# Kernel optimization log

Measured on AMD Instinct MI355X. Metric: run time of the kernel, lower is better.

The kernel has to match this reference:

```python
import jax, jax.numpy as jnp
import numpy as np

WINDOW = 128
CAUSAL = True
LOOK_BACKWARD = 1
LOOK_FORWARD = 0  # causal forces look_forward = 0


def _look_around(x, backward, forward, pad_value, dim):
    # pad along window axis (axis=1), then concat shifted slices along `dim`
    nw = x.shape[1]
    pad_cfg = [(0, 0)] * x.ndim
    pad_cfg[1] = (backward, forward)
    padded = jnp.pad(x, pad_cfg, constant_values=pad_value)
    slices = [padded[:, i:i + nw] for i in range(forward + backward + 1)]
    return jnp.concatenate(slices, axis=dim)


def setup_inputs() -> dict:
    key = jax.random.key(0)
    kq, kk, kv = jax.random.split(key, 3)
    shape = (2, 16, 4096, 64)
    return {
        "q": jax.random.normal(kq, shape, dtype=jnp.float32),
        "k": jax.random.normal(kk, shape, dtype=jnp.float32),
        "v": jax.random.normal(kv, shape, dtype=jnp.float32),
    }


def reference(q, k, v):
    b, h, t, e = q.shape
    scale = e ** (-0.5)
    windows = t // WINDOW  # t assumed divisible by WINDOW (pad_to_multiple is no-op)

    # merge batch and heads, bucket into windows
    bq = q.reshape(b * h, windows, WINDOW, e)
    bk = k.reshape(b * h, windows, WINDOW, e)
    bv = v.reshape(b * h, windows, WINDOW, e)

    # look-around gather of key/value windows: j-dim = WINDOW*(1+back+fwd)
    bk = _look_around(bk, LOOK_BACKWARD, LOOK_FORWARD, 0.0, dim=2)
    bv = _look_around(bv, LOOK_BACKWARD, LOOK_FORWARD, 0.0, dim=2)

    # positional indices for masking
    bq_t = jnp.arange(t).reshape(1, windows, WINDOW)
    bq_k = _look_around(bq_t, LOOK_BACKWARD, LOOK_FORWARD, -1, dim=2)

    mask = (bq_k == -1)[:, :, None, :]  # (1, w, 1, j) padded positions
    if CAUSAL:
        mask = mask | (bq_t[:, :, :, None] < bq_k[:, :, None, :])

    dots = jnp.einsum('bwie,bwje->bwij', bq * scale, bk)
    mask_value = -jnp.finfo(dots.dtype).max
    dots = jnp.where(mask, mask_value, dots)
    attn = jax.nn.softmax(dots.astype(jnp.float32), axis=-1).astype(dots.dtype)
    out = jnp.einsum('bwij,bwje->bwie', attn, bv)
    return out.reshape(b, h, t, e)
```

## Files before the change

kernel.cpp:

```cpp
#include <hip/hip_runtime.h>

#define T_DIM 4096
#define E_DIM 64
#define WIN   128
#define NWIN  (T_DIM / WIN)
#define KS_LD 72
#define VT_LD 136
#define PS_LD 36

typedef __bf16  bf16x8 __attribute__((ext_vector_type(8)));
typedef __bf16  bf16x4 __attribute__((ext_vector_type(4)));
typedef float   f32x16 __attribute__((ext_vector_type(16)));

template<int CTRL>
__device__ __forceinline__ float dppf(float x) {
  return __int_as_float(__builtin_amdgcn_update_dpp(0, __float_as_int(x), CTRL, 0xf, 0xf, false));
}
__device__ __forceinline__ float rsum32(float x) {
  x += dppf<0xB1>(x);
  x += dppf<0x4E>(x);
  x += dppf<0x141>(x);
  x += dppf<0x140>(x);
  x += __int_as_float(__builtin_amdgcn_ds_swizzle(__float_as_int(x), 0x401F));
  return x;
}

__global__ __launch_bounds__(256, 3)
void la_fwd(const float* __restrict__ Q, const float* __restrict__ K,
            const float* __restrict__ V, float* __restrict__ O)
{
  __shared__ __bf16 Ks[WIN * KS_LD];
  __shared__ __bf16 Vt[E_DIM * VT_LD];
  __shared__ __bf16 Psm[4 * 32 * PS_LD];

  const int tid  = threadIdx.x;
  const int lane = tid & 63;
  const int wid  = tid >> 6;
  const int col  = lane & 31;
  const int half = lane >> 5;

  const int w  = blockIdx.x;
  const int bh = blockIdx.y;

  const float* Qb = Q + (size_t)bh * T_DIM * E_DIM;
  const float* Kb = K + (size_t)bh * T_DIM * E_DIM;
  const float* Vb = V + (size_t)bh * T_DIM * E_DIM;
  float*       Ob = O + (size_t)bh * T_DIM * E_DIM;

  const int q0 = w * WIN;

  const float QS = 0.125f * 1.44269504088896340736f;
  bf16x8 aq[4];
  {
    const float* qrow = Qb + (size_t)(q0 + wid * 32 + col) * E_DIM;
#pragma unroll
    for (int c = 0; c < 4; ++c) {
      const float* p = qrow + c * 16 + half * 8;
      const float4 x = *(const float4*)(p);
      const float4 y = *(const float4*)(p + 4);
      bf16x8 a;
      a[0]=(__bf16)(x.x*QS); a[1]=(__bf16)(x.y*QS); a[2]=(__bf16)(x.z*QS); a[3]=(__bf16)(x.w*QS);
      a[4]=(__bf16)(y.x*QS); a[5]=(__bf16)(y.y*QS); a[6]=(__bf16)(y.z*QS); a[7]=(__bf16)(y.w*QS);
      aq[c] = a;
    }
  }

  float lr[16];
  f32x16 oacc[2];
#pragma unroll
  for (int r = 0; r < 16; ++r) lr[r] = 0.0f;
#pragma unroll
  for (int et = 0; et < 2; ++et)
#pragma unroll
    for (int r = 0; r < 16; ++r) oacc[et][r] = 0.0f;

  __bf16* Ps = Psm + wid * (32 * PS_LD);

  auto stage = [&](int kr0) {
    const float* kp = Kb + (size_t)kr0 * E_DIM;
#pragma unroll 4
    for (int i = 0; i < 8; ++i) {
      const int fi = (i << 10) + (tid << 2);
      const float4 kv = *(const float4*)(kp + fi);
      const int row = fi >> 6, cole = fi & 63;
      bf16x4 k4; k4[0]=(__bf16)kv.x; k4[1]=(__bf16)kv.y; k4[2]=(__bf16)kv.z; k4[3]=(__bf16)kv.w;
      *(bf16x4*)(&Ks[row * KS_LD + cole]) = k4;
    }
    const int j  = tid & 127;
    const int ch = (tid >> 7) * 32;
    const float* vrow = Vb + (size_t)(kr0 + j) * E_DIM + ch;
#pragma unroll 4
    for (int c4 = 0; c4 < 8; ++c4) {
      const float4 vv = *(const float4*)(vrow + c4 * 4);
      const int e = ch + c4 * 4;
      Vt[(e + 0) * VT_LD + j] = (__bf16)vv.x;
      Vt[(e + 1) * VT_LD + j] = (__bf16)vv.y;
      Vt[(e + 2) * VT_LD + j] = (__bf16)vv.z;
      Vt[(e + 3) * VT_LD + j] = (__bf16)vv.w;
    }
  };

  auto kb_step = [&](int kb, bool diag) {
    f32x16 s;
#pragma unroll
    for (int r = 0; r < 16; ++r) s[r] = 0.0f;
#pragma unroll
    for (int c = 0; c < 4; ++c) {
      const bf16x8 bk = *(const bf16x8*)(&Ks[(kb * 32 + col) * KS_LD + c * 16 + half * 8]);
      s = __builtin_amdgcn_mfma_f32_32x32x16_bf16(aq[c], bk, s, 0, 0, 0);
    }
#pragma unroll
    for (int r = 0; r < 16; ++r) {
      const int row = (r & 3) + 8 * (r >> 2) + 4 * half;
      float sv = s[r];
      if (diag && col > row) sv = -3.0e38f;
      const float p = __builtin_amdgcn_exp2f(sv);
      lr[r] += p;
      Ps[row * PS_LD + col] = (__bf16)p;
    }
    bf16x8 ap[2];
#pragma unroll
    for (int c2 = 0; c2 < 2; ++c2) {
      const __bf16* rp = Ps + col * PS_LD + c2 * 16 + half * 8;
      union { bf16x8 v8; bf16x4 v4[2]; } u;
      u.v4[0] = *(const bf16x4*)(rp);
      u.v4[1] = *(const bf16x4*)(rp + 4);
      ap[c2] = u.v8;
    }
#pragma unroll
    for (int c2 = 0; c2 < 2; ++c2) {
      const int j0 = kb * 32 + c2 * 16 + half * 8;
#pragma unroll
      for (int et = 0; et < 2; ++et) {
        const bf16x8 bv = *(const bf16x8*)(&Vt[(et * 32 + col) * VT_LD + j0]);
        oacc[et] = __builtin_amdgcn_mfma_f32_32x32x16_bf16(ap[c2], bv, oacc[et], 0, 0, 0);
      }
    }
  };

  if (w > 0) {
    stage(q0 - WIN);
    __syncthreads();
#pragma unroll
    for (int kb = 0; kb < 4; ++kb) kb_step(kb, false);
    __syncthreads();
  }

  stage(q0);
  __syncthreads();
  for (int kb = 0; kb <= wid; ++kb) kb_step(kb, kb == wid);

#pragma unroll
  for (int r = 0; r < 16; ++r) {
    const int row  = (r & 3) + 8 * (r >> 2) + 4 * half;
    const float rinv = __builtin_amdgcn_rcpf(rsum32(lr[r]));
    float* op = Ob + (size_t)(q0 + wid * 32 + row) * E_DIM;
    op[col]      = oacc[0][r] * rinv;
    op[col + 32] = oacc[1][r] * rinv;
  }
}

extern "C" void kernel_launch(void* const* d_in, const int* in_sizes, int n_in,
                              void* d_out, int out_size, void* d_ws, size_t ws_size,
                              hipStream_t stream) {
  const float* Q = (const float*)d_in[0];
  const float* K = (const float*)d_in[1];
  const float* V = (const float*)d_in[2];
  float*       O = (float*)d_out;
  const int bh = in_sizes[0] / (T_DIM * E_DIM);
  dim3 grid(NWIN, bh);
  la_fwd<<<grid, 256, 0, stream>>>(Q, K, V, O);
}
```

Before: 146.4 us.

## Stage both K/V windows up front into separate LDS buffers

Gives K and V two LDS buffers each and loads the previous window and the current window together before a single barrier, instead of stage-sync-compute-sync-stage-sync. This cuts two block barriers and lets the global loads for both windows be in flight at once. In exchange LDS use per block roughly doubles and the launch bound drops from 3 to 2 blocks per CU, which lowers occupancy.

```diff
diff --git a/kernel.cpp b/kernel.cpp
--- a/kernel.cpp
+++ b/kernel.cpp
@@ -25,12 +25,12 @@
   return x;
 }
 
-__global__ __launch_bounds__(256, 3)
+__global__ __launch_bounds__(256, 2)
 void la_fwd(const float* __restrict__ Q, const float* __restrict__ K,
             const float* __restrict__ V, float* __restrict__ O)
 {
-  __shared__ __bf16 Ks[WIN * KS_LD];
-  __shared__ __bf16 Vt[E_DIM * VT_LD];
+  __shared__ __bf16 Ks[2][WIN * KS_LD];
+  __shared__ __bf16 Vt[2][E_DIM * VT_LD];
   __shared__ __bf16 Psm[4 * 32 * PS_LD];
 
   const int tid  = threadIdx.x;
@@ -65,6 +65,32 @@
     }
   }
 
+  auto stage = [&](int kr0, int buf) {
+    const float* kp = Kb + (size_t)kr0 * E_DIM;
+    __bf16* ks = Ks[buf];
+    __bf16* vt = Vt[buf];
+#pragma unroll 4
+    for (int i = 0; i < 8; ++i) {
+      const int fi = (i << 10) + (tid << 2);
+      const float4 kv = *(const float4*)(kp + fi);
+      const int row = fi >> 6, cole = fi & 63;
+      bf16x4 k4; k4[0]=(__bf16)kv.x; k4[1]=(__bf16)kv.y; k4[2]=(__bf16)kv.z; k4[3]=(__bf16)kv.w;
+      *(bf16x4*)(&ks[row * KS_LD + cole]) = k4;
+    }
+    const int j  = tid & 127;
+    const int ch = (tid >> 7) * 32;
+    const float* vrow = Vb + (size_t)(kr0 + j) * E_DIM + ch;
+#pragma unroll 4
+    for (int c4 = 0; c4 < 8; ++c4) {
+      const float4 vv = *(const float4*)(vrow + c4 * 4);
+      const int e = ch + c4 * 4;
+      vt[(e + 0) * VT_LD + j] = (__bf16)vv.x;
+      vt[(e + 1) * VT_LD + j] = (__bf16)vv.y;
+      vt[(e + 2) * VT_LD + j] = (__bf16)vv.z;
+      vt[(e + 3) * VT_LD + j] = (__bf16)vv.w;
+    }
+  };
+
   float lr[16];
   f32x16 oacc[2];
 #pragma unroll
@@ -76,37 +102,13 @@
 
   __bf16* Ps = Psm + wid * (32 * PS_LD);
 
-  auto stage = [&](int kr0) {
-    const float* kp = Kb + (size_t)kr0 * E_DIM;
-#pragma unroll 4
-    for (int i = 0; i < 8; ++i) {
-      const int fi = (i << 10) + (tid << 2);
-      const float4 kv = *(const float4*)(kp + fi);
-      const int row = fi >> 6, cole = fi & 63;
-      bf16x4 k4; k4[0]=(__bf16)kv.x; k4[1]=(__bf16)kv.y; k4[2]=(__bf16)kv.z; k4[3]=(__bf16)kv.w;
-      *(bf16x4*)(&Ks[row * KS_LD + cole]) = k4;
-    }
-    const int j  = tid & 127;
-    const int ch = (tid >> 7) * 32;
-    const float* vrow = Vb + (size_t)(kr0 + j) * E_DIM + ch;
-#pragma unroll 4
-    for (int c4 = 0; c4 < 8; ++c4) {
-      const float4 vv = *(const float4*)(vrow + c4 * 4);
-      const int e = ch + c4 * 4;
-      Vt[(e + 0) * VT_LD + j] = (__bf16)vv.x;
-      Vt[(e + 1) * VT_LD + j] = (__bf16)vv.y;
-      Vt[(e + 2) * VT_LD + j] = (__bf16)vv.z;
-      Vt[(e + 3) * VT_LD + j] = (__bf16)vv.w;
-    }
-  };
-
-  auto kb_step = [&](int kb, bool diag) {
+  auto kb_step = [&](int kb, bool diag, int buf) {
     f32x16 s;
 #pragma unroll
     for (int r = 0; r < 16; ++r) s[r] = 0.0f;
 #pragma unroll
     for (int c = 0; c < 4; ++c) {
-      const bf16x8 bk = *(const bf16x8*)(&Ks[(kb * 32 + col) * KS_LD + c * 16 + half * 8]);
+      const bf16x8 bk = *(const bf16x8*)(&Ks[buf][(kb * 32 + col) * KS_LD + c * 16 + half * 8]);
       s = __builtin_amdgcn_mfma_f32_32x32x16_bf16(aq[c], bk, s, 0, 0, 0);
     }
 #pragma unroll
@@ -132,23 +134,21 @@
       const int j0 = kb * 32 + c2 * 16 + half * 8;
 #pragma unroll
       for (int et = 0; et < 2; ++et) {
-        const bf16x8 bv = *(const bf16x8*)(&Vt[(et * 32 + col) * VT_LD + j0]);
+        const bf16x8 bv = *(const bf16x8*)(&Vt[buf][(et * 32 + col) * VT_LD + j0]);
         oacc[et] = __builtin_amdgcn_mfma_f32_32x32x16_bf16(ap[c2], bv, oacc[et], 0, 0, 0);
       }
     }
   };
 
+  if (w > 0) stage(q0 - WIN, 0);
+  stage(q0, 1);
+  __syncthreads();
+
   if (w > 0) {
-    stage(q0 - WIN);
-    __syncthreads();
 #pragma unroll
-    for (int kb = 0; kb < 4; ++kb) kb_step(kb, false);
-    __syncthreads();
+    for (int kb = 0; kb < 4; ++kb) kb_step(kb, false, 0);
   }
-
-  stage(q0);
-  __syncthreads();
-  for (int kb = 0; kb <= wid; ++kb) kb_step(kb, kb == wid);
+  for (int kb = 0; kb <= wid; ++kb) kb_step(kb, kb == wid, 1);
 
 #pragma unroll
   for (int r = 0; r < 16; ++r) {
```

Result: no change. 147.2 us (+0.6%).

## Compute transposed scores to keep P in registers via permlane32 swap

Applied to the files above, without the earlier changes.

Swaps the MFMA operand order so each lane holds one query's scores across keys. The probabilities can then be repacked to bf16 and exchanged between the two 32-lane halves with permlane32_swap, which removes the per-warp LDS staging of P. The per-row sum becomes a single scalar combined with one shuffle at the end. Outputs are stored as float4 rows, and launch bounds rise to 4 blocks per CU. The risk is higher register pressure under the tighter occupancy target.

```diff
diff --git a/kernel.cpp b/kernel.cpp
--- a/kernel.cpp
+++ b/kernel.cpp
@@ -6,32 +6,33 @@
 #define NWIN  (T_DIM / WIN)
 #define KS_LD 72
 #define VT_LD 136
-#define PS_LD 36
 
 typedef __bf16  bf16x8 __attribute__((ext_vector_type(8)));
 typedef __bf16  bf16x4 __attribute__((ext_vector_type(4)));
 typedef float   f32x16 __attribute__((ext_vector_type(16)));
 
-template<int CTRL>
-__device__ __forceinline__ float dppf(float x) {
-  return __int_as_float(__builtin_amdgcn_update_dpp(0, __float_as_int(x), CTRL, 0xf, 0xf, false));
+#if defined(__has_builtin) && __has_builtin(__builtin_amdgcn_permlane32_swap)
+typedef int v2i_t __attribute__((ext_vector_type(2)));
+__device__ __forceinline__ void lane32_swap(unsigned &a, unsigned &b) {
+  v2i_t r = __builtin_amdgcn_permlane32_swap((int)a, (int)b, false, false);
+  a = (unsigned)r.x; b = (unsigned)r.y;
 }
-__device__ __forceinline__ float rsum32(float x) {
-  x += dppf<0xB1>(x);
-  x += dppf<0x4E>(x);
-  x += dppf<0x141>(x);
-  x += dppf<0x140>(x);
-  x += __int_as_float(__builtin_amdgcn_ds_swizzle(__float_as_int(x), 0x401F));
-  return x;
+#else
+__device__ __forceinline__ void lane32_swap(unsigned &a, unsigned &b) {
+  const bool lo = ((threadIdx.x & 63) < 32);
+  const unsigned pa = __shfl_xor(a, 32), pb = __shfl_xor(b, 32);
+  const unsigned na = lo ? a : pb;
+  const unsigned nb = lo ? pa : b;
+  a = na; b = nb;
 }
+#endif
 
-__global__ __launch_bounds__(256, 3)
+__global__ __launch_bounds__(256, 4)
 void la_fwd(const float* __restrict__ Q, const float* __restrict__ K,
             const float* __restrict__ V, float* __restrict__ O)
 {
   __shared__ __bf16 Ks[WIN * KS_LD];
   __shared__ __bf16 Vt[E_DIM * VT_LD];
-  __shared__ __bf16 Psm[4 * 32 * PS_LD];
 
   const int tid  = threadIdx.x;
   const int lane = tid & 63;
@@ -65,16 +66,12 @@
     }
   }
 
-  float lr[16];
+  float lr = 0.0f;
   f32x16 oacc[2];
-#pragma unroll
-  for (int r = 0; r < 16; ++r) lr[r] = 0.0f;
 #pragma unroll
   for (int et = 0; et < 2; ++et)
 #pragma unroll
     for (int r = 0; r < 16; ++r) oacc[et][r] = 0.0f;
-
-  __bf16* Ps = Psm + wid * (32 * PS_LD);
 
   auto stage = [&](int kr0) {
     const float* kp = Kb + (size_t)kr0 * E_DIM;
@@ -106,34 +103,39 @@
     for (int r = 0; r < 16; ++r) s[r] = 0.0f;
 #pragma unroll
     for (int c = 0; c < 4; ++c) {
-      const bf16x8 bk = *(const bf16x8*)(&Ks[(kb * 32 + col) * KS_LD + c * 16 + half * 8]);
-      s = __builtin_amdgcn_mfma_f32_32x32x16_bf16(aq[c], bk, s, 0, 0, 0);
+      const bf16x8 ak = *(const bf16x8*)(&Ks[(kb * 32 + col) * KS_LD + c * 16 + half * 8]);
+      s = __builtin_amdgcn_mfma_f32_32x32x16_bf16(ak, aq[c], s, 0, 0, 0);
     }
 #pragma unroll
     for (int r = 0; r < 16; ++r) {
-      const int row = (r & 3) + 8 * (r >> 2) + 4 * half;
+      const int kk = (r & 3) + 8 * (r >> 2) + 4 * half;
       float sv = s[r];
-      if (diag && col > row) sv = -3.0e38f;
+      if (diag && kk > col) sv = -3.0e38f;
       const float p = __builtin_amdgcn_exp2f(sv);
-      lr[r] += p;
-      Ps[row * PS_LD + col] = (__bf16)p;
+      lr += p;
+      s[r] = p;
     }
-    bf16x8 ap[2];
+    unsigned pk8[8];
 #pragma unroll
-    for (int c2 = 0; c2 < 2; ++c2) {
-      const __bf16* rp = Ps + col * PS_LD + c2 * 16 + half * 8;
-      union { bf16x8 v8; bf16x4 v4[2]; } u;
-      u.v4[0] = *(const bf16x4*)(rp);
-      u.v4[1] = *(const bf16x4*)(rp + 4);
-      ap[c2] = u.v8;
+    for (int g = 0; g < 8; ++g) {
+      union { __bf16 h[2]; unsigned u; } pu;
+      pu.h[0] = (__bf16)s[2 * g];
+      pu.h[1] = (__bf16)s[2 * g + 1];
+      pk8[g] = pu.u;
     }
 #pragma unroll
     for (int c2 = 0; c2 < 2; ++c2) {
+      unsigned b0 = pk8[4 * c2 + 0], b1 = pk8[4 * c2 + 1];
+      unsigned b2 = pk8[4 * c2 + 2], b3 = pk8[4 * c2 + 3];
+      lane32_swap(b0, b2);
+      lane32_swap(b1, b3);
+      union { unsigned u[4]; bf16x8 v; } bf;
+      bf.u[0] = b0; bf.u[1] = b1; bf.u[2] = b2; bf.u[3] = b3;
       const int j0 = kb * 32 + c2 * 16 + half * 8;
 #pragma unroll
       for (int et = 0; et < 2; ++et) {
-        const bf16x8 bv = *(const bf16x8*)(&Vt[(et * 32 + col) * VT_LD + j0]);
-        oacc[et] = __builtin_amdgcn_mfma_f32_32x32x16_bf16(ap[c2], bv, oacc[et], 0, 0, 0);
+        const bf16x8 av = *(const bf16x8*)(&Vt[(et * 32 + col) * VT_LD + j0]);
+        oacc[et] = __builtin_amdgcn_mfma_f32_32x32x16_bf16(av, bf.v, oacc[et], 0, 0, 0);
       }
     }
   };
@@ -150,14 +152,20 @@
   __syncthreads();
   for (int kb = 0; kb <= wid; ++kb) kb_step(kb, kb == wid);
 
+  const float ltot = lr + __shfl_xor(lr, 32);
+  const float rinv = __builtin_amdgcn_rcpf(ltot);
+  float* op = Ob + (size_t)(q0 + wid * 32 + col) * E_DIM;
 #pragma unroll
-  for (int r = 0; r < 16; ++r) {
-    const int row  = (r & 3) + 8 * (r >> 2) + 4 * half;
-    const float rinv = __builtin_amdgcn_rcpf(rsum32(lr[r]));
-    float* op = Ob + (size_t)(q0 + wid * 32 + row) * E_DIM;
-    op[col]      = oacc[0][r] * rinv;
-    op[col + 32] = oacc[1][r] * rinv;
-  }
+  for (int et = 0; et < 2; ++et)
+#pragma unroll
+    for (int g = 0; g < 4; ++g) {
+      float4 o4;
+      o4.x = oacc[et][4 * g + 0] * rinv;
+      o4.y = oacc[et][4 * g + 1] * rinv;
+      o4.z = oacc[et][4 * g + 2] * rinv;
+      o4.w = oacc[et][4 * g + 3] * rinv;
+      *(float4*)(op + et * 32 + 8 * g + 4 * half) = o4;
+    }
 }
 
 extern "C" void kernel_launch(void* const* d_in, const int* in_sizes, int n_in,
```

Result: no change. 147.6 us (+0.9%).
